# Performance work log

Measured on AMD Instinct MI355X. Metric: run time of the kernel, lower is better.

The kernel has to match this reference:

```python
import jax, jax.numpy as jnp
import numpy as np

EPS = 1e-12  # matches NTMNet epsilon


def setup_inputs() -> dict:
    key = jax.random.key(0)
    ks = jax.random.split(key, 12)
    B, L, C, D, H = 64, 16384, 64, 256, 100
    F = D + 1 * C  # inputs concat flattened reading (1 reader)
    def w(k, shape):
        return jax.random.normal(k, shape, dtype=jnp.float32) * 0.05
    return {
        "inputs": w(ks[0], (B, D)),
        "reading": w(ks[1], (B, 1, C)),
        "memory": w(ks[2], (B, L, C)),
        "W1": w(ks[3], (F, H)), "b1": jnp.zeros((H,), jnp.float32),
        "W2": w(ks[4], (H, H)), "b2": jnp.zeros((H,), jnp.float32),
        "Wk_r": w(ks[5], (H, C)), "bk_r": jnp.zeros((C,), jnp.float32),
        "Ws_r": w(ks[6], (H, 1)), "bs_r": jnp.zeros((1,), jnp.float32),
        "Wk_w": w(ks[7], (H, C)), "bk_w": jnp.zeros((C,), jnp.float32),
        "Ws_w": w(ks[8], (H, 1)), "bs_w": jnp.zeros((1,), jnp.float32),
        "We": w(ks[9], (H, C)), "be": jnp.zeros((C,), jnp.float32),
        "Wa": w(ks[10], (H, C)), "ba": jnp.zeros((C,), jnp.float32),
    }


def reference(inputs, reading, memory, W1, b1, W2, b2,
              Wk_r, bk_r, Ws_r, bs_r, Wk_w, bk_w, Ws_w, bs_w,
              We, be, Wa, ba):
    B = inputs.shape[0]
    feat = jnp.concatenate([inputs, reading.reshape(B, -1)], axis=-1)
    h = jnp.tanh(jnp.tanh(feat @ W1 + b1) @ W2 + b2)  # [B,H]

    # memory normalized over the whole (lines, cols) matrix per batch element
    mnorm = jnp.sqrt(jnp.sum(memory * memory, axis=(-2, -1), keepdims=True))
    mem_n = memory / jnp.maximum(mnorm, EPS)  # [B,L,C]

    def addressing(Wk, bk, Ws, bs):
        # content addressing: cosine-sim of key vs memory rows, sharpened softmax
        kvec = h @ Wk + bk  # [B,C] (no activation)
        kvec = kvec / jnp.maximum(jnp.linalg.norm(kvec, axis=1, keepdims=True), EPS)
        s = jax.nn.sigmoid(h @ Ws + bs)  # [B,1] strength
        K = jnp.einsum('blc,bc->bl', mem_n, kvec)  # [B,L]
        return jax.nn.softmax(K * s, axis=-1)  # [B,L]

    # read head
    w_r = addressing(Wk_r, bk_r, Ws_r, bs_r)
    read = jnp.einsum('bl,blc->bc', w_r, memory)  # [B,C]

    # write head: erase then add
    w_w = addressing(Wk_w, bk_w, Ws_w, bs_w)
    e = jax.nn.sigmoid(h @ We + be)  # [B,C]
    a = jax.nn.sigmoid(h @ Wa + ba)  # [B,C]
    ww = w_w[:, :, None]  # [B,L,1]
    new_mem = memory * (1.0 - ww * e[:, None, :]) + ww * a[:, None, :]  # [B,L,C]
    return read, new_mem
```

## Files before the change

kernel.cpp:

```cpp
#include <hip/hip_runtime.h>
#include <math.h>

#define B 64
#define L 16384
#define C 64
#define D 256
#define H 100
#define F 320
#define EPSV 1e-12f
#define CHUNKS 32
#define RPC 512

typedef float nfloat4 __attribute__((ext_vector_type(4)));

__device__ inline float waveReduceSum(float v) {
    v += __shfl_xor(v, 32);
    v += __shfl_xor(v, 16);
    v += __shfl_xor(v, 8);
    v += __shfl_xor(v, 4);
    v += __shfl_xor(v, 2);
    v += __shfl_xor(v, 1);
    return v;
}

__global__ __launch_bounds__(256) void k1_kernel(
    const float* __restrict__ inputs, const float* __restrict__ reading,
    const float* __restrict__ mem,
    const float* __restrict__ W1, const float* __restrict__ b1,
    const float* __restrict__ W2, const float* __restrict__ b2,
    const float* __restrict__ Wk_r, const float* __restrict__ bk_r,
    const float* __restrict__ Ws_r, const float* __restrict__ bs_r,
    const float* __restrict__ Wk_w, const float* __restrict__ bk_w,
    const float* __restrict__ Ws_w, const float* __restrict__ bs_w,
    const float* __restrict__ We, const float* __restrict__ be,
    const float* __restrict__ Wa, const float* __restrict__ ba,
    float* __restrict__ kv_r, float* __restrict__ kv_w,
    float* __restrict__ ev, float* __restrict__ av,
    float* __restrict__ s_r, float* __restrict__ s_w,
    float* __restrict__ partial_ss)
{
    const int g = blockIdx.x;
    const int t = threadIdx.x;

    if (g < B * CHUNKS) {
        const int b = g >> 5, chunk = g & 31;
        const int wave = t >> 6, lane = t & 63;
        const int sub = lane >> 4, m = lane & 15;
        const float4* memv = (const float4*)(mem + (size_t)b * L * C);
        float lss = 0.f;
        const int row0 = chunk * RPC;
        #pragma unroll 8
        for (int it = 0; it < 32; ++it) {
            const int row = row0 + it * 16 + wave * 4 + sub;
            const float4 v = memv[row * 16 + m];
            lss = fmaf(v.x, v.x, fmaf(v.y, v.y, fmaf(v.z, v.z, fmaf(v.w, v.w, lss))));
        }
        lss = waveReduceSum(lss);
        __shared__ float wsum[4];
        if (lane == 0) wsum[wave] = lss;
        __syncthreads();
        if (t == 0) partial_ss[g] = wsum[0] + wsum[1] + wsum[2] + wsum[3];
    } else {
        const int b = g - B * CHUNKS;
        __shared__ float feat[F];
        __shared__ float h1[H], h2[H];
        __shared__ float kr_s[C], kw_s[C], ee_s[C], aa_s[C];
        __shared__ float invs[2];

        feat[t] = inputs[b * D + t];
        if (t < C) feat[D + t] = reading[b * C + t];
        __syncthreads();
        if (t < H) {
            float acc = b1[t];
            for (int f = 0; f < F; ++f) acc += feat[f] * W1[f * H + t];
            h1[t] = tanhf(acc);
        }
        __syncthreads();
        if (t < H) {
            float acc = b2[t];
            for (int k = 0; k < H; ++k) acc += h1[k] * W2[k * H + t];
            h2[t] = tanhf(acc);
        }
        __syncthreads();
        if (t < C) {
            float a0 = bk_r[t], a1 = bk_w[t], a2 = be[t], a3 = ba[t];
            for (int j = 0; j < H; ++j) {
                const float hv = h2[j];
                a0 += hv * Wk_r[j * C + t];
                a1 += hv * Wk_w[j * C + t];
                a2 += hv * We[j * C + t];
                a3 += hv * Wa[j * C + t];
            }
            kr_s[t] = a0; kw_s[t] = a1;
            ee_s[t] = 1.f / (1.f + expf(-a2));
            aa_s[t] = 1.f / (1.f + expf(-a3));
        } else if (t == 64 || t == 65) {
            const float* Ws = (t == 64) ? Ws_r : Ws_w;
            float acc = (t == 64) ? bs_r[0] : bs_w[0];
            for (int j = 0; j < H; ++j) acc += h2[j] * Ws[j];
            const float s = 1.f / (1.f + expf(-acc));
            if (t == 64) s_r[b] = s; else s_w[b] = s;
        }
        __syncthreads();
        if (t < 64) {
            const float xr = kr_s[t], xw = kw_s[t];
            const float nr = waveReduceSum(xr * xr);
            const float nw = waveReduceSum(xw * xw);
            if (t == 0) {
                invs[0] = 1.f / fmaxf(sqrtf(nr), EPSV);
                invs[1] = 1.f / fmaxf(sqrtf(nw), EPSV);
            }
        }
        __syncthreads();
        if (t < C) {
            kv_r[b * C + t] = kr_s[t] * invs[0];
            kv_w[b * C + t] = kw_s[t] * invs[1];
            ev[b * C + t] = ee_s[t];
            av[b * C + t] = aa_s[t];
        }
    }
}

__global__ __launch_bounds__(256) void k2_kernel(
    const float* __restrict__ mem,
    const float* __restrict__ kv_r, const float* __restrict__ kv_w,
    const float* __restrict__ s_r, const float* __restrict__ s_w,
    const float* __restrict__ partial_ss,
    float* __restrict__ partial_S, float* __restrict__ out_read)
{
    const int b = blockIdx.y;
    const int chunk = blockIdx.x;
    const int t = threadIdx.x;
    const int wave = t >> 6, lane = t & 63;
    const int sub = lane >> 4, m = lane & 15;

    if (chunk == 0 && t < C) out_read[b * C + t] = 0.f;

    __shared__ float sc_sh[2];
    if (t < 64) {
        float p = (t < CHUNKS) ? partial_ss[b * CHUNKS + t] : 0.f;
        p = waveReduceSum(p);
        if (t == 0) {
            const float invn = 1.f / fmaxf(sqrtf(p), EPSV);
            sc_sh[0] = s_r[b] * invn;
            sc_sh[1] = s_w[b] * invn;
        }
    }
    __syncthreads();
    const float sc_r = sc_sh[0], sc_w = sc_sh[1];

    const float4 kr = *(const float4*)(kv_r + b * C + m * 4);
    const float4 kw = *(const float4*)(kv_w + b * C + m * 4);
    const float4* memv = (const float4*)(mem + (size_t)b * L * C);

    float er = 0.f, ew = 0.f;
    const int row0 = chunk * RPC;
    #pragma unroll 4
    for (int it = 0; it < 32; ++it) {
        const int row = row0 + it * 16 + wave * 4 + sub;
        const float4 v = memv[row * 16 + m];
        float pr = v.x * kr.x + v.y * kr.y + v.z * kr.z + v.w * kr.w;
        float pw = v.x * kw.x + v.y * kw.y + v.z * kw.z + v.w * kw.w;
        pr += __shfl_xor(pr, 1);
        pw += __shfl_xor(pw, 1);
        float x = (m & 1) ? pw : pr;
        x += __shfl_xor(x, 2);
        x += __shfl_xor(x, 4);
        x += __shfl_xor(x, 8);
        const float y = __shfl_xor(x, 1);
        if (m == 0) {
            er += expf(x * sc_r);
            ew += expf(y * sc_w);
        }
    }
    er = waveReduceSum(er);
    ew = waveReduceSum(ew);
    __shared__ float wr_sh[4], ww_sh[4];
    if (lane == 0) { wr_sh[wave] = er; ww_sh[wave] = ew; }
    __syncthreads();
    if (t == 0) {
        float* ps = partial_S + (size_t)(b * CHUNKS + chunk) * 2;
        ps[0] = wr_sh[0] + wr_sh[1] + wr_sh[2] + wr_sh[3];
        ps[1] = ww_sh[0] + ww_sh[1] + ww_sh[2] + ww_sh[3];
    }
}

__global__ __launch_bounds__(256) void k3_kernel(
    const float* __restrict__ mem,
    const float* __restrict__ kv_r, const float* __restrict__ kv_w,
    const float* __restrict__ s_r, const float* __restrict__ s_w,
    const float* __restrict__ partial_ss, const float* __restrict__ partial_S,
    const float* __restrict__ ev, const float* __restrict__ av,
    float* __restrict__ out_read, float* __restrict__ new_mem)
{
    const int b = blockIdx.y;
    const int chunk = blockIdx.x;
    const int t = threadIdx.x;
    const int wave = t >> 6, lane = t & 63;
    const int sub = lane >> 4, m = lane & 15;

    __shared__ float tmp_sh[3];
    __shared__ float st_sh[4];
    if (wave == 0) {
        float p = (lane < CHUNKS) ? partial_ss[b * CHUNKS + lane] : 0.f;
        p = waveReduceSum(p);
        if (lane == 0) tmp_sh[0] = p;
    } else if (wave == 1) {
        float p = (lane < CHUNKS) ? partial_S[(size_t)(b * CHUNKS + lane) * 2] : 0.f;
        p = waveReduceSum(p);
        if (lane == 0) tmp_sh[1] = p;
    } else if (wave == 2) {
        float p = (lane < CHUNKS) ? partial_S[(size_t)(b * CHUNKS + lane) * 2 + 1] : 0.f;
        p = waveReduceSum(p);
        if (lane == 0) tmp_sh[2] = p;
    }
    __syncthreads();
    if (t == 0) {
        const float invn = 1.f / fmaxf(sqrtf(tmp_sh[0]), EPSV);
        st_sh[0] = s_r[b] * invn;
        st_sh[1] = s_w[b] * invn;
        st_sh[2] = 1.f / tmp_sh[1];
        st_sh[3] = 1.f / tmp_sh[2];
    }
    __syncthreads();
    const float sc_r = st_sh[0], sc_w = st_sh[1];
    const float inv_r = st_sh[2], inv_w = st_sh[3];

    const float4 kr = *(const float4*)(kv_r + b * C + m * 4);
    const float4 kw = *(const float4*)(kv_w + b * C + m * 4);
    const float4 e4 = *(const float4*)(ev + b * C + m * 4);
    const float4 a4 = *(const float4*)(av + b * C + m * 4);
    const float4* memv = (const float4*)(mem + (size_t)b * L * C);
    nfloat4* outv = (nfloat4*)(new_mem + (size_t)b * L * C);

    float4 racc = {0.f, 0.f, 0.f, 0.f};
    const int row0 = chunk * RPC;
    #pragma unroll 4
    for (int it = 0; it < 32; ++it) {
        const int row = row0 + it * 16 + wave * 4 + sub;
        const float4 v = memv[row * 16 + m];
        float pr = v.x * kr.x + v.y * kr.y + v.z * kr.z + v.w * kr.w;
        float pw = v.x * kw.x + v.y * kw.y + v.z * kw.z + v.w * kw.w;
        pr += __shfl_xor(pr, 1);
        pw += __shfl_xor(pw, 1);
        float x = (m & 1) ? pw : pr;
        x += __shfl_xor(x, 2);
        x += __shfl_xor(x, 4);
        x += __shfl_xor(x, 8);
        const float y = __shfl_xor(x, 1);
        const float dr = (m & 1) ? y : x;
        const float dw = (m & 1) ? x : y;
        const float wr = expf(dr * sc_r) * inv_r;
        const float ww = expf(dw * sc_w) * inv_w;
        nfloat4 nm;
        nm.x = v.x * (1.f - ww * e4.x) + ww * a4.x;
        nm.y = v.y * (1.f - ww * e4.y) + ww * a4.y;
        nm.z = v.z * (1.f - ww * e4.z) + ww * a4.z;
        nm.w = v.w * (1.f - ww * e4.w) + ww * a4.w;
        __builtin_nontemporal_store(nm, &outv[row * 16 + m]);
        racc.x = fmaf(wr, v.x, racc.x);
        racc.y = fmaf(wr, v.y, racc.y);
        racc.z = fmaf(wr, v.z, racc.z);
        racc.w = fmaf(wr, v.w, racc.w);
    }
    racc.x += __shfl_xor(racc.x, 16); racc.x += __shfl_xor(racc.x, 32);
    racc.y += __shfl_xor(racc.y, 16); racc.y += __shfl_xor(racc.y, 32);
    racc.z += __shfl_xor(racc.z, 16); racc.z += __shfl_xor(racc.z, 32);
    racc.w += __shfl_xor(racc.w, 16); racc.w += __shfl_xor(racc.w, 32);
    __shared__ float lds[4][64];
    if (lane < 16) {
        lds[wave][m * 4 + 0] = racc.x;
        lds[wave][m * 4 + 1] = racc.y;
        lds[wave][m * 4 + 2] = racc.z;
        lds[wave][m * 4 + 3] = racc.w;
    }
    __syncthreads();
    if (t < 64) {
        const float tot = lds[0][t] + lds[1][t] + lds[2][t] + lds[3][t];
        atomicAdd(&out_read[b * C + t], tot);
    }
}

extern "C" void kernel_launch(void* const* d_in, const int* in_sizes, int n_in,
                              void* d_out, int out_size, void* d_ws, size_t ws_size,
                              hipStream_t stream) {
    const float* inputs  = (const float*)d_in[0];
    const float* reading = (const float*)d_in[1];
    const float* memory  = (const float*)d_in[2];
    const float* W1 = (const float*)d_in[3];
    const float* b1 = (const float*)d_in[4];
    const float* W2 = (const float*)d_in[5];
    const float* b2 = (const float*)d_in[6];
    const float* Wk_r = (const float*)d_in[7];
    const float* bk_r = (const float*)d_in[8];
    const float* Ws_r = (const float*)d_in[9];
    const float* bs_r = (const float*)d_in[10];
    const float* Wk_w = (const float*)d_in[11];
    const float* bk_w = (const float*)d_in[12];
    const float* Ws_w = (const float*)d_in[13];
    const float* bs_w = (const float*)d_in[14];
    const float* We = (const float*)d_in[15];
    const float* be = (const float*)d_in[16];
    const float* Wa = (const float*)d_in[17];
    const float* ba = (const float*)d_in[18];

    float* ws = (float*)d_ws;
    float* kv_r       = ws;
    float* kv_w       = ws + 4096;
    float* ev         = ws + 8192;
    float* av         = ws + 12288;
    float* s_r        = ws + 16384;
    float* s_w        = ws + 16448;
    float* partial_ss = ws + 16512;
    float* partial_S  = ws + 18560;

    float* out = (float*)d_out;
    float* out_read = out;
    float* new_mem  = out + 4096;

    k1_kernel<<<B * CHUNKS + B, 256, 0, stream>>>(
        inputs, reading, memory, W1, b1, W2, b2,
        Wk_r, bk_r, Ws_r, bs_r, Wk_w, bk_w, Ws_w, bs_w,
        We, be, Wa, ba,
        kv_r, kv_w, ev, av, s_r, s_w, partial_ss);

    k2_kernel<<<dim3(CHUNKS, B), 256, 0, stream>>>(
        memory, kv_r, kv_w, s_r, s_w, partial_ss, partial_S, out_read);

    k3_kernel<<<dim3(CHUNKS, B), 256, 0, stream>>>(
        memory, kv_r, kv_w, s_r, s_w, partial_ss, partial_S,
        ev, av, out_read, new_mem);
}
```

Measured before the change: 580.1 us.

## Fuse memory norm and dot products into one pass, cache dots for later stages

The first kernel now computes the controller per block, then in one pass over memory accumulates the squared norm and writes the raw read/write key dot products per row to a workspace buffer. A single-block-per-batch kernel reduces the softmax denominators from these cached dots. The final kernel reuses the dots instead of recomputing them, which removes one full pass over memory. In exchange, the controller MLP is computed redundantly by every chunk block, adding serial latency before each block starts streaming.

```diff
diff --git a/kernel.cpp b/kernel.cpp
--- a/kernel.cpp
+++ b/kernel.cpp
@@ -34,126 +34,80 @@
     const float* __restrict__ Ws_w, const float* __restrict__ bs_w,
     const float* __restrict__ We, const float* __restrict__ be,
     const float* __restrict__ Wa, const float* __restrict__ ba,
-    float* __restrict__ kv_r, float* __restrict__ kv_w,
     float* __restrict__ ev, float* __restrict__ av,
     float* __restrict__ s_r, float* __restrict__ s_w,
-    float* __restrict__ partial_ss)
+    float* __restrict__ partial_ss, float2* __restrict__ dot2)
 {
     const int g = blockIdx.x;
-    const int t = threadIdx.x;
-
-    if (g < B * CHUNKS) {
-        const int b = g >> 5, chunk = g & 31;
-        const int wave = t >> 6, lane = t & 63;
-        const int sub = lane >> 4, m = lane & 15;
-        const float4* memv = (const float4*)(mem + (size_t)b * L * C);
-        float lss = 0.f;
-        const int row0 = chunk * RPC;
-        #pragma unroll 8
-        for (int it = 0; it < 32; ++it) {
-            const int row = row0 + it * 16 + wave * 4 + sub;
-            const float4 v = memv[row * 16 + m];
-            lss = fmaf(v.x, v.x, fmaf(v.y, v.y, fmaf(v.z, v.z, fmaf(v.w, v.w, lss))));
-        }
-        lss = waveReduceSum(lss);
-        __shared__ float wsum[4];
-        if (lane == 0) wsum[wave] = lss;
-        __syncthreads();
-        if (t == 0) partial_ss[g] = wsum[0] + wsum[1] + wsum[2] + wsum[3];
-    } else {
-        const int b = g - B * CHUNKS;
-        __shared__ float feat[F];
-        __shared__ float h1[H], h2[H];
-        __shared__ float kr_s[C], kw_s[C], ee_s[C], aa_s[C];
-        __shared__ float invs[2];
-
-        feat[t] = inputs[b * D + t];
-        if (t < C) feat[D + t] = reading[b * C + t];
-        __syncthreads();
-        if (t < H) {
-            float acc = b1[t];
-            for (int f = 0; f < F; ++f) acc += feat[f] * W1[f * H + t];
-            h1[t] = tanhf(acc);
-        }
-        __syncthreads();
-        if (t < H) {
-            float acc = b2[t];
-            for (int k = 0; k < H; ++k) acc += h1[k] * W2[k * H + t];
-            h2[t] = tanhf(acc);
-        }
-        __syncthreads();
-        if (t < C) {
-            float a0 = bk_r[t], a1 = bk_w[t], a2 = be[t], a3 = ba[t];
-            for (int j = 0; j < H; ++j) {
-                const float hv = h2[j];
-                a0 += hv * Wk_r[j * C + t];
-                a1 += hv * Wk_w[j * C + t];
-                a2 += hv * We[j * C + t];
-                a3 += hv * Wa[j * C + t];
-            }
-            kr_s[t] = a0; kw_s[t] = a1;
-            ee_s[t] = 1.f / (1.f + expf(-a2));
-            aa_s[t] = 1.f / (1.f + expf(-a3));
-        } else if (t == 64 || t == 65) {
-            const float* Ws = (t == 64) ? Ws_r : Ws_w;
-            float acc = (t == 64) ? bs_r[0] : bs_w[0];
-            for (int j = 0; j < H; ++j) acc += h2[j] * Ws[j];
-            const float s = 1.f / (1.f + expf(-acc));
-            if (t == 64) s_r[b] = s; else s_w[b] = s;
-        }
-        __syncthreads();
-        if (t < 64) {
-            const float xr = kr_s[t], xw = kw_s[t];
-            const float nr = waveReduceSum(xr * xr);
-            const float nw = waveReduceSum(xw * xw);
-            if (t == 0) {
-                invs[0] = 1.f / fmaxf(sqrtf(nr), EPSV);
-                invs[1] = 1.f / fmaxf(sqrtf(nw), EPSV);
-            }
-        }
-        __syncthreads();
-        if (t < C) {
-            kv_r[b * C + t] = kr_s[t] * invs[0];
-            kv_w[b * C + t] = kw_s[t] * invs[1];
-            ev[b * C + t] = ee_s[t];
-            av[b * C + t] = aa_s[t];
-        }
-    }
-}
-
-__global__ __launch_bounds__(256) void k2_kernel(
-    const float* __restrict__ mem,
-    const float* __restrict__ kv_r, const float* __restrict__ kv_w,
-    const float* __restrict__ s_r, const float* __restrict__ s_w,
-    const float* __restrict__ partial_ss,
-    float* __restrict__ partial_S, float* __restrict__ out_read)
-{
-    const int b = blockIdx.y;
-    const int chunk = blockIdx.x;
+    const int b = g >> 5, chunk = g & 31;
     const int t = threadIdx.x;
     const int wave = t >> 6, lane = t & 63;
     const int sub = lane >> 4, m = lane & 15;
 
-    if (chunk == 0 && t < C) out_read[b * C + t] = 0.f;
-
-    __shared__ float sc_sh[2];
-    if (t < 64) {
-        float p = (t < CHUNKS) ? partial_ss[b * CHUNKS + t] : 0.f;
-        p = waveReduceSum(p);
+    __shared__ float feat[F];
+    __shared__ float h1[H], h2[H];
+    __shared__ float kr_s[C], kw_s[C];
+    __shared__ float invs[2];
+
+    feat[t] = inputs[b * D + t];
+    if (t < C) feat[D + t] = reading[b * C + t];
+    __syncthreads();
+    if (t < H) {
+        float acc = b1[t];
+        for (int f = 0; f < F; ++f) acc += feat[f] * W1[f * H + t];
+        h1[t] = tanhf(acc);
+    }
+    __syncthreads();
+    if (t < H) {
+        float acc = b2[t];
+        for (int k = 0; k < H; ++k) acc += h1[k] * W2[k * H + t];
+        h2[t] = tanhf(acc);
+    }
+    __syncthreads();
+    if (t < C) {
+        float a0 = bk_r[t], a1 = bk_w[t], a2 = be[t], a3 = ba[t];
+        for (int j = 0; j < H; ++j) {
+            const float hv = h2[j];
+            a0 += hv * Wk_r[j * C + t];
+            a1 += hv * Wk_w[j * C + t];
+            a2 += hv * We[j * C + t];
+            a3 += hv * Wa[j * C + t];
+        }
+        kr_s[t] = a0; kw_s[t] = a1;
+        if (chunk == 0) {
+            ev[b * C + t] = 1.f / (1.f + expf(-a2));
+            av[b * C + t] = 1.f / (1.f + expf(-a3));
+        }
+    } else if (t == 64 || t == 65) {
+        const float* Ws = (t == 64) ? Ws_r : Ws_w;
+        float acc = (t == 64) ? bs_r[0] : bs_w[0];
+        for (int j = 0; j < H; ++j) acc += h2[j] * Ws[j];
+        const float s = 1.f / (1.f + expf(-acc));
+        if (chunk == 0) { if (t == 64) s_r[b] = s; else s_w[b] = s; }
+    }
+    __syncthreads();
+    if (t < 64) {
+        const float xr = kr_s[t], xw = kw_s[t];
+        const float nr = waveReduceSum(xr * xr);
+        const float nw = waveReduceSum(xw * xw);
         if (t == 0) {
-            const float invn = 1.f / fmaxf(sqrtf(p), EPSV);
-            sc_sh[0] = s_r[b] * invn;
-            sc_sh[1] = s_w[b] * invn;
-        }
-    }
-    __syncthreads();
-    const float sc_r = sc_sh[0], sc_w = sc_sh[1];
-
-    const float4 kr = *(const float4*)(kv_r + b * C + m * 4);
-    const float4 kw = *(const float4*)(kv_w + b * C + m * 4);
+            invs[0] = 1.f / fmaxf(sqrtf(nr), EPSV);
+            invs[1] = 1.f / fmaxf(sqrtf(nw), EPSV);
+        }
+    }
+    __syncthreads();
+    if (t < 64) {
+        kr_s[t] *= invs[0];
+        kw_s[t] *= invs[1];
+    }
+    __syncthreads();
+
+    const float4 kr = *(const float4*)(kr_s + m * 4);
+    const float4 kw = *(const float4*)(kw_s + m * 4);
     const float4* memv = (const float4*)(mem + (size_t)b * L * C);
-
-    float er = 0.f, ew = 0.f;
+    float2* d2 = dot2 + (size_t)b * L;
+
+    float lss = 0.f;
     const int row0 = chunk * RPC;
     #pragma unroll 4
     for (int it = 0; it < 32; ++it) {
@@ -161,6 +115,7 @@
         const float4 v = memv[row * 16 + m];
         float pr = v.x * kr.x + v.y * kr.y + v.z * kr.z + v.w * kr.w;
         float pw = v.x * kw.x + v.y * kw.y + v.z * kw.z + v.w * kw.w;
+        lss = fmaf(v.x, v.x, fmaf(v.y, v.y, fmaf(v.z, v.z, fmaf(v.w, v.w, lss))));
         pr += __shfl_xor(pr, 1);
         pw += __shfl_xor(pw, 1);
         float x = (m & 1) ? pw : pr;
@@ -168,28 +123,66 @@
         x += __shfl_xor(x, 4);
         x += __shfl_xor(x, 8);
         const float y = __shfl_xor(x, 1);
-        if (m == 0) {
-            er += expf(x * sc_r);
-            ew += expf(y * sc_w);
-        }
+        if (m == 0) d2[row] = make_float2(x, y);
+    }
+    lss = waveReduceSum(lss);
+    __shared__ float wsum[4];
+    if (lane == 0) wsum[wave] = lss;
+    __syncthreads();
+    if (t == 0) partial_ss[g] = wsum[0] + wsum[1] + wsum[2] + wsum[3];
+}
+
+__global__ __launch_bounds__(1024) void k2_kernel(
+    const float2* __restrict__ dot2,
+    const float* __restrict__ s_r, const float* __restrict__ s_w,
+    const float* __restrict__ partial_ss,
+    float* __restrict__ stats, float* __restrict__ out_read)
+{
+    const int b = blockIdx.x;
+    const int t = threadIdx.x;
+    const int wave = t >> 6, lane = t & 63;
+
+    if (t < C) out_read[b * C + t] = 0.f;
+
+    __shared__ float sc_sh[2];
+    if (t < 64) {
+        float p = (t < CHUNKS) ? partial_ss[b * CHUNKS + t] : 0.f;
+        p = waveReduceSum(p);
+        if (t == 0) {
+            const float invn = 1.f / fmaxf(sqrtf(p), EPSV);
+            sc_sh[0] = s_r[b] * invn;
+            sc_sh[1] = s_w[b] * invn;
+        }
+    }
+    __syncthreads();
+    const float sc_r = sc_sh[0], sc_w = sc_sh[1];
+
+    const float2* p = dot2 + (size_t)b * L;
+    float er = 0.f, ew = 0.f;
+    #pragma unroll
+    for (int k = 0; k < 16; ++k) {
+        const float2 d = p[t + k * 1024];
+        er += expf(d.x * sc_r);
+        ew += expf(d.y * sc_w);
     }
     er = waveReduceSum(er);
     ew = waveReduceSum(ew);
-    __shared__ float wr_sh[4], ww_sh[4];
-    if (lane == 0) { wr_sh[wave] = er; ww_sh[wave] = ew; }
+    __shared__ float redr[16], redw[16];
+    if (lane == 0) { redr[wave] = er; redw[wave] = ew; }
     __syncthreads();
     if (t == 0) {
-        float* ps = partial_S + (size_t)(b * CHUNKS + chunk) * 2;
-        ps[0] = wr_sh[0] + wr_sh[1] + wr_sh[2] + wr_sh[3];
-        ps[1] = ww_sh[0] + ww_sh[1] + ww_sh[2] + ww_sh[3];
+        float a = 0.f, c = 0.f;
+        for (int i = 0; i < 16; ++i) { a += redr[i]; c += redw[i]; }
+        float* st = stats + b * 8;
+        st[0] = sc_r; st[1] = 1.f / a;
+        st[2] = sc_w; st[3] = 1.f / c;
     }
 }
 
 __global__ __launch_bounds__(256) void k3_kernel(
     const float* __restrict__ mem,
-    const float* __restrict__ kv_r, const float* __restrict__ kv_w,
-    const float* __restrict__ s_r, const float* __restrict__ s_w,
-    const float* __restrict__ partial_ss, const float* __restrict__ partial_S,
+    const float2* __restrict__ dot2,
+    const float* __restrict__ stats,
     const float* __restrict__ ev, const float* __restrict__ av,
     float* __restrict__ out_read, float* __restrict__ new_mem)
 {
@@ -199,59 +192,23 @@
     const int wave = t >> 6, lane = t & 63;
     const int sub = lane >> 4, m = lane & 15;
 
-    __shared__ float tmp_sh[3];
-    __shared__ float st_sh[4];
-    if (wave == 0) {
-        float p = (lane < CHUNKS) ? partial_ss[b * CHUNKS + lane] : 0.f;
-        p = waveReduceSum(p);
-        if (lane == 0) tmp_sh[0] = p;
-    } else if (wave == 1) {
-        float p = (lane < CHUNKS) ? partial_S[(size_t)(b * CHUNKS + lane) * 2] : 0.f;
-        p = waveReduceSum(p);
-        if (lane == 0) tmp_sh[1] = p;
-    } else if (wave == 2) {
-        float p = (lane < CHUNKS) ? partial_S[(size_t)(b * CHUNKS + lane) * 2 + 1] : 0.f;
-        p = waveReduceSum(p);
-        if (lane == 0) tmp_sh[2] = p;
-    }
-    __syncthreads();
-    if (t == 0) {
-        const float invn = 1.f / fmaxf(sqrtf(tmp_sh[0]), EPSV);
-        st_sh[0] = s_r[b] * invn;
-        st_sh[1] = s_w[b] * invn;
-        st_sh[2] = 1.f / tmp_sh[1];
-        st_sh[3] = 1.f / tmp_sh[2];
-    }
-    __syncthreads();
-    const float sc_r = st_sh[0], sc_w = st_sh[1];
-    const float inv_r = st_sh[2], inv_w = st_sh[3];
-
-    const float4 kr = *(const float4*)(kv_r + b * C + m * 4);
-    const float4 kw = *(const float4*)(kv_w + b * C + m * 4);
+    const float4 st4 = *(const float4*)(stats + b * 8);
+    const float sc_r = st4.x, inv_r = st4.y, sc_w = st4.z, inv_w = st4.w;
     const float4 e4 = *(const float4*)(ev + b * C + m * 4);
     const float4 a4 = *(const float4*)(av + b * C + m * 4);
     const float4* memv = (const float4*)(mem + (size_t)b * L * C);
     nfloat4* outv = (nfloat4*)(new_mem + (size_t)b * L * C);
+    const float2* d2 = dot2 + (size_t)b * L;
 
     float4 racc = {0.f, 0.f, 0.f, 0.f};
     const int row0 = chunk * RPC;
     #pragma unroll 4
     for (int it = 0; it < 32; ++it) {
         const int row = row0 + it * 16 + wave * 4 + sub;
+        const float2 d = d2[row];
+        const float wr = expf(d.x * sc_r) * inv_r;
+        const float ww = expf(d.y * sc_w) * inv_w;
         const float4 v = memv[row * 16 + m];
-        float pr = v.x * kr.x + v.y * kr.y + v.z * kr.z + v.w * kr.w;
-        float pw = v.x * kw.x + v.y * kw.y + v.z * kw.z + v.w * kw.w;
-        pr += __shfl_xor(pr, 1);
-        pw += __shfl_xor(pw, 1);
-        float x = (m & 1) ? pw : pr;
-        x += __shfl_xor(x, 2);
-        x += __shfl_xor(x, 4);
-        x += __shfl_xor(x, 8);
-        const float y = __shfl_xor(x, 1);
-        const float dr = (m & 1) ? y : x;
-        const float dw = (m & 1) ? x : y;
-        const float wr = expf(dr * sc_r) * inv_r;
-        const float ww = expf(dw * sc_w) * inv_w;
         nfloat4 nm;
         nm.x = v.x * (1.f - ww * e4.x) + ww * a4.x;
         nm.y = v.y * (1.f - ww * e4.y) + ww * a4.y;
@@ -305,29 +262,27 @@
     const float* ba = (const float*)d_in[18];
 
     float* ws = (float*)d_ws;
-    float* kv_r       = ws;
-    float* kv_w       = ws + 4096;
-    float* ev         = ws + 8192;
-    float* av         = ws + 12288;
-    float* s_r        = ws + 16384;
-    float* s_w        = ws + 16448;
-    float* partial_ss = ws + 16512;
-    float* partial_S  = ws + 18560;
+    float* ev         = ws;
+    float* av         = ws + 4096;
+    float* s_r        = ws + 8192;
+    float* s_w        = ws + 8256;
+    float* partial_ss = ws + 8320;
+    float* stats      = ws + 10368;
+    float2* dot2      = (float2*)(ws + 11264);
 
     float* out = (float*)d_out;
     float* out_read = out;
     float* new_mem  = out + 4096;
 
-    k1_kernel<<<B * CHUNKS + B, 256, 0, stream>>>(
+    k1_kernel<<<B * CHUNKS, 256, 0, stream>>>(
         inputs, reading, memory, W1, b1, W2, b2,
         Wk_r, bk_r, Ws_r, bs_r, Wk_w, bk_w, Ws_w, bs_w,
         We, be, Wa, ba,
-        kv_r, kv_w, ev, av, s_r, s_w, partial_ss);
-
-    k2_kernel<<<dim3(CHUNKS, B), 256, 0, stream>>>(
-        memory, kv_r, kv_w, s_r, s_w, partial_ss, partial_S, out_read);
+        ev, av, s_r, s_w, partial_ss, dot2);
+
+    k2_kernel<<<B, 1024, 0, stream>>>(
+        dot2, s_r, s_w, partial_ss, stats, out_read);
 
     k3_kernel<<<dim3(CHUNKS, B), 256, 0, stream>>>(
-        memory, kv_r, kv_w, s_r, s_w, partial_ss, partial_S,
-        ev, av, out_read, new_mem);
-}
+        memory, dot2, stats, ev, av, out_read, new_mem);
+}
```

Result: faster. 565.2 us (-2.6%).
